# Performance work log

Measured on AMD Instinct MI355X. Metric: run time of the kernel, lower is better.

Reference implementation:

```python
import jax, jax.numpy as jnp
import numpy as np

EMB = 2048
HEADS = 16


def setup_inputs() -> dict:
    key = jax.random.key(0)
    k_x, k_wqkv, k_bqkv, k_wo, k_bo = jax.random.split(key, 5)
    B, S, E = 2, 2048, EMB
    x = jax.random.normal(k_x, (B, S, E), dtype=jnp.float32)
    # nn.Linear weights stored as (in, out) for x @ W + b convention
    W_qkv = jax.random.normal(k_wqkv, (E, 3 * E), dtype=jnp.float32) * 0.02
    b_qkv = jax.random.normal(k_bqkv, (3 * E,), dtype=jnp.float32) * 0.02
    W_out = jax.random.normal(k_wo, (E, E), dtype=jnp.float32) * 0.02
    b_out = jax.random.normal(k_bo, (E,), dtype=jnp.float32) * 0.02
    return {"x": x, "W_qkv": W_qkv, "b_qkv": b_qkv, "W_out": W_out, "b_out": b_out}


def reference(x, W_qkv, b_qkv, W_out, b_out):
    B, S, E = x.shape
    H = HEADS
    dh = E // H
    # QKV projection: (B,S,3E)
    qkv = x @ W_qkv + b_qkv
    # Faithful to torch: reshape (B,S,H,3*dh) THEN split -> interleaved per-head q/k/v
    qkv = qkv.reshape(B, S, H, 3 * dh).transpose(0, 2, 1, 3)  # (B,H,S,3*dh)
    q, k, v = jnp.split(qkv, 3, axis=-1)  # each (B,H,S,dh)
    q = q / jnp.asarray(dh, q.dtype) ** 0.5
    scores = jnp.einsum('bhqd,bhkd->bhqk', q, k)  # (B,H,S,S)
    weights = jax.nn.softmax(scores, axis=-1)
    attn = jnp.einsum('bhqk,bhkd->bhqd', weights, v)  # (B,H,S,dh)
    attn = attn.transpose(0, 2, 1, 3).reshape(B, S, E)
    return attn @ W_out + b_out
```

## Files before the change

kernel.cpp:

```cpp
#include <hip/hip_runtime.h>
#include <type_traits>
#include <utility>

#define DI __device__ __forceinline__

typedef unsigned short u16;
typedef float f32x4 __attribute__((ext_vector_type(4)));
typedef float f32x16 __attribute__((ext_vector_type(16)));
typedef short s16x8 __attribute__((ext_vector_type(8)));
typedef __bf16 bf16x8 __attribute__((ext_vector_type(8)));

template <typename V, typename = void>
struct mfma_ok : std::false_type {};
template <typename V>
struct mfma_ok<V, std::void_t<decltype(__builtin_amdgcn_mfma_f32_16x16x32_bf16(
    std::declval<V>(), std::declval<V>(), std::declval<f32x4>(), 0, 0, 0))>>
    : std::true_type {};
using frag_t = std::conditional_t<mfma_ok<bf16x8>::value, bf16x8, s16x8>;

union U128 {
  int4 i;
  frag_t f;
  u16 s[8];
};

DI f32x4 mfma16(const U128& a, const U128& b, f32x4 c) {
  return __builtin_amdgcn_mfma_f32_16x16x32_bf16(a.f, b.f, c, 0, 0, 0);
}
DI f32x16 mfma32(const U128& a, const U128& b, f32x16 c) {
  return __builtin_amdgcn_mfma_f32_32x32x16_bf16(a.f, b.f, c, 0, 0, 0);
}

DI u16 f2b(float x) {
  union { float f; unsigned u; } v; v.f = x;
  unsigned r = v.u + 0x7FFFu + ((v.u >> 16) & 1u);
  return (u16)(r >> 16);
}

DI unsigned pk2bf(float a, float b) {
  unsigned short ua = __builtin_bit_cast(unsigned short, (__bf16)a);
  unsigned short ub = __builtin_bit_cast(unsigned short, (__bf16)b);
  return (unsigned)ua | ((unsigned)ub << 16);
}

#if __has_builtin(__builtin_amdgcn_exp2f)
#define EXP2F __builtin_amdgcn_exp2f
#else
#define EXP2F exp2f
#endif

DI void plswap(unsigned& lo, unsigned& hi) {
  asm("v_permlane32_swap_b32 %0, %1" : "+v"(lo), "+v"(hi));
}

typedef __attribute__((address_space(1))) void gas_t;
typedef __attribute__((address_space(3))) void las_t;
DI void gll16(const void* g, void* l) {
  __builtin_amdgcn_global_load_lds((gas_t*)g, (las_t*)l, 16, 0, 0);
}

#define QSCALE 0.12751791437603762f

DI void transpose_tile(const float* __restrict__ in, u16* __restrict__ out,
                       int R, int C, int bx, int by, int t, u16 (*Tb)[68]) {
  long r0 = (long)by * 64, c0 = (long)bx * 64;
  int cq = (t & 15) * 4, rr = t >> 4;
#pragma unroll
  for (int it = 0; it < 4; ++it) {
    int r = rr + it * 16;
    float4 v = *(const float4*)(in + (r0 + r) * C + c0 + cq);
    Tb[r][cq + 0] = f2b(v.x); Tb[r][cq + 1] = f2b(v.y);
    Tb[r][cq + 2] = f2b(v.z); Tb[r][cq + 3] = f2b(v.w);
  }
  __syncthreads();
#pragma unroll
  for (int it = 0; it < 2; ++it) {
    int ci = it * 256 + t;
    int cc = ci >> 3, ch = ci & 7, rb = ch * 8;
    unsigned p0 = Tb[rb + 0][cc] | ((unsigned)Tb[rb + 1][cc] << 16);
    unsigned p1 = Tb[rb + 2][cc] | ((unsigned)Tb[rb + 3][cc] << 16);
    unsigned p2 = Tb[rb + 4][cc] | ((unsigned)Tb[rb + 5][cc] << 16);
    unsigned p3 = Tb[rb + 6][cc] | ((unsigned)Tb[rb + 7][cc] << 16);
    *(int4*)(out + (c0 + cc) * R + r0 + rb) = make_int4(p0, p1, p2, p3);
  }
}

__global__ __launch_bounds__(256) void k_pre(const float* __restrict__ x,
                                             u16* __restrict__ xb,
                                             const float* __restrict__ Wqkv,
                                             u16* __restrict__ wqkvt) {
  __shared__ __attribute__((aligned(16))) u16 Tb[64][68];
  int bid = blockIdx.x, t = threadIdx.x;
  if (bid < 8192) {
    int i = bid * 256 + t;
    float4 v = ((const float4*)x)[i];
    ushort4 o;
    o.x = f2b(v.x); o.y = f2b(v.y); o.z = f2b(v.z); o.w = f2b(v.w);
    ((ushort4*)xb)[i] = o;
    return;
  }
  int idx = bid - 8192;
  transpose_tile(Wqkv, wqkvt, 2048, 6144, idx % 96, idx / 96, t, Tb);
}

template <int MODE>
__global__ __launch_bounds__(256, 4) void k_gemm_bt(const u16* __restrict__ A,
                                                    const u16* __restrict__ Bt,
                                                    const float* __restrict__ bias,
                                                    void* __restrict__ Cout,
                                                    u16* __restrict__ qb,
                                                    u16* __restrict__ kbv,
                                                    u16* __restrict__ vt,
                                                    int n_off,
                                                    int M, int N, int K) {
  __shared__ __attribute__((aligned(16))) u16 SM[16384];
  u16* As = SM;
  u16* Bs = SM + 8192;
  int t = threadIdx.x;
  int lane = t & 63, w = t >> 6, quad = lane >> 4, l15 = lane & 15;
  long m0 = (long)blockIdx.y * 128, n0 = n_off + (long)blockIdx.x * 128;
  int wr = (w >> 1) * 64, wc = (w & 1) * 64;
  int sw = l15 & 7;
  f32x4 acc[4][4] = {};
  for (int k0 = 0; k0 < K; k0 += 64) {
    __syncthreads();
#pragma unroll
    for (int it = 0; it < 4; ++it) {
      int ci = it * 256 + t;
      int row = ci >> 3, cl = (ci & 7) ^ (row & 7);
      gll16(A + (m0 + row) * K + k0 + cl * 8, As + ci * 8);
      gll16(Bt + (n0 + row) * K + k0 + cl * 8, Bs + ci * 8);
    }
    __syncthreads();
#pragma unroll
    for (int kk = 0; kk < 2; ++kk) {
      U128 a[4], b[4];
#pragma unroll
      for (int i = 0; i < 4; ++i)
        a[i].i = *(const int4*)(As + (wr + i * 16 + l15) * 64 + (((kk * 4 + quad) ^ sw) << 3));
#pragma unroll
      for (int j = 0; j < 4; ++j)
        b[j].i = *(const int4*)(Bs + (wc + j * 16 + l15) * 64 + (((kk * 4 + quad) ^ sw) << 3));
#pragma unroll
      for (int i = 0; i < 4; ++i)
#pragma unroll
        for (int j = 0; j < 4; ++j)
          acc[i][j] = mfma16(a[i], b[j], acc[i][j]);
    }
  }
  float bj[4];
#pragma unroll
  for (int j = 0; j < 4; ++j) bj[j] = bias[n0 + wc + j * 16 + l15];

  int hidx = (int)(n0 / 384);
  int rsel = (int)(n0 - hidx * 384) >> 7;

  if (MODE == 1 && rsel == 2) {
    __syncthreads();
#pragma unroll
    for (int i = 0; i < 4; ++i)
#pragma unroll
      for (int rr2 = 0; rr2 < 4; ++rr2) {
        int m = wr + i * 16 + quad * 4 + rr2;
#pragma unroll
        for (int j = 0; j < 4; ++j)
          SM[m * 128 + wc + j * 16 + l15] = f2b(acc[i][j][rr2] + bj[j]);
      }
    __syncthreads();
    int bidx = (int)(m0 >> 11), s0 = (int)(m0 & 2047);
    u16* vrow = vt + (long)(bidx * 16 + hidx) * 128 * 2048 + s0;
#pragma unroll
    for (int it = 0; it < 8; ++it) {
      int ci = it * 256 + t;
      int d = ci & 127, sb = (ci >> 7) * 8;
      unsigned p0 = SM[(sb + 0) * 128 + d] | ((unsigned)SM[(sb + 1) * 128 + d] << 16);
      unsigned p1 = SM[(sb + 2) * 128 + d] | ((unsigned)SM[(sb + 3) * 128 + d] << 16);
      unsigned p2 = SM[(sb + 4) * 128 + d] | ((unsigned)SM[(sb + 5) * 128 + d] << 16);
      unsigned p3 = SM[(sb + 6) * 128 + d] | ((unsigned)SM[(sb + 7) * 128 + d] << 16);
      *(int4*)(vrow + (long)d * 2048 + sb) = make_int4(p0, p1, p2, p3);
    }
    return;
  }

  u16* route = (MODE == 1) ? (rsel == 0 ? qb : kbv) : nullptr;

#pragma unroll
  for (int i = 0; i < 4; ++i) {
#pragma unroll
    for (int rr2 = 0; rr2 < 4; ++rr2) {
      long row = m0 + wr + i * 16 + quad * 4 + rr2;
#pragma unroll
      for (int j = 0; j < 4; ++j) {
        float v = acc[i][j][rr2] + bj[j];
        if (MODE == 1) {
          if (rsel == 0) v *= QSCALE;
          int bidx = (int)(row >> 11), s = (int)(row & 2047);
          long obase = ((long)(bidx * 16 + hidx) * 2048 + s) * 128;
          int dh = wc + j * 16 + l15;
          unsigned pb = f2b(v);
          unsigned other = __shfl_xor(pb, 1);
          if (!(l15 & 1))
            ((unsigned*)route)[(obase + dh) >> 1] = pb | (other << 16);
        } else {
          long col = n0 + wc + j * 16 + l15;
          unsigned bits = __float_as_uint(v);
          unsigned other = __shfl_xor(bits, 1);
          if (!(l15 & 1)) {
            uint2 pr; pr.x = bits; pr.y = other;
            *(uint2*)((float*)Cout + row * N + col) = pr;
          }
        }
      }
    }
  }
}

__global__ __launch_bounds__(256, 2) void k_flash(const u16* __restrict__ qb,
                                                  const u16* __restrict__ kb,
                                                  const u16* __restrict__ vt,
                                                  u16* __restrict__ attn,
                                                  const float* __restrict__ Wout,
                                                  u16* __restrict__ woutt) {
  __shared__ __attribute__((aligned(16))) u16 Ks[2][64 * 128];
  __shared__ __attribute__((aligned(16))) u16 Vts[2][128 * 64];
  if (blockIdx.y >= 32) {
    u16 (*Tb)[68] = (u16(*)[68])(&Ks[0][0]);
    int u = (blockIdx.y - 32) * 16 + blockIdx.x;
    transpose_tile(Wout, woutt, 2048, 2048, u & 31, u >> 5, threadIdx.x, Tb);
    return;
  }
  int t = threadIdx.x;
  int lane = t & 63, w = t >> 6, l31 = lane & 31, h = lane >> 5;
  int q0 = blockIdx.x * 128 + w * 32;
  int bh = blockIdx.y, b = bh >> 4, hd = bh & 15;

  const u16* qbase = qb + ((long)bh * 2048 + q0 + l31) * 128;
  U128 qf[8];
#pragma unroll
  for (int dht = 0; dht < 8; ++dht)
    qf[dht].i = *(const int4*)(qbase + dht * 16 + h * 8);
  __syncthreads();

  f32x16 O[4] = {};
  float ls0 = 0.f, ls1 = 0.f, ls2 = 0.f, ls3 = 0.f;
  const u16* kbh = kb + (long)bh * 2048 * 128;
  long vbase = (long)bh * 128 * 2048;

  unsigned swx = (unsigned)(((l31 & 7) << 3) ^ (h << 3));
  unsigned kinv = ((unsigned)l31 << 7) ^ swx;
  unsigned vinv = ((unsigned)l31 << 6) ^ swx;

  auto stage = [&](int buf, int k0) {
#pragma unroll
    for (int it = 0; it < 4; ++it) {
      int ci = it * 256 + t;
      int key = ci >> 4, cp = ci & 15, cl = cp ^ (key & 7);
      gll16(kbh + (long)(k0 + key) * 128 + cl * 8, &Ks[buf][0] + ci * 8);
    }
#pragma unroll
    for (int it = 0; it < 4; ++it) {
      int ci = it * 256 + t;
      int d = ci >> 3, cp = ci & 7, cl = cp ^ (d & 7);
      gll16(vt + vbase + (long)d * 2048 + k0 + cl * 8, &Vts[buf][0] + ci * 8);
    }
  };

  stage(0, 0);
  int cur = 0;
  for (int k0 = 0; k0 < 2048; k0 += 64) {
    if (k0 + 64 < 2048) {
      stage(cur ^ 1, k0 + 64);
      asm volatile("s_waitcnt vmcnt(8)" ::: "memory");
    } else {
      asm volatile("s_waitcnt vmcnt(0)" ::: "memory");
    }
    __builtin_amdgcn_s_barrier();
    asm volatile("" ::: "memory");
    const u16* KbT = &Ks[cur][0];
    const u16* VbT = &Vts[cur][0];

    f32x16 St0 = {}, St1 = {};
    __builtin_amdgcn_s_setprio(1);
#pragma unroll
    for (int dht = 0; dht < 8; ++dht) {
      U128 kf;
      kf.i = *(const int4*)(KbT + (kinv ^ (unsigned)(dht << 4)));
      St0 = mfma32(kf, qf[dht], St0);
    }
#pragma unroll
    for (int dht = 0; dht < 8; ++dht) {
      U128 kf;
      kf.i = *(const int4*)(KbT + (kinv ^ (unsigned)(dht << 4)) + 4096);
      St1 = mfma32(kf, qf[dht], St1);
    }
    __builtin_amdgcn_s_setprio(0);

    auto pv = [&](int kt, const U128& pfk) {
#pragma unroll
      for (int dht = 0; dht < 4; ++dht) {
        U128 vf;
        vf.i = *(const int4*)(VbT + (vinv ^ (unsigned)(kt << 4)) + dht * 2048);
        O[dht] = mfma32(vf, pfk, O[dht]);
      }
    };
    auto mkpf = [&](const float* p) {
      unsigned w0 = pk2bf(p[0], p[1]);
      unsigned w1 = pk2bf(p[2], p[3]);
      unsigned w2 = pk2bf(p[4], p[5]);
      unsigned w3 = pk2bf(p[6], p[7]);
      plswap(w0, w2);
      plswap(w1, w3);
      U128 r; r.i = make_int4(w0, w1, w2, w3);
      return r;
    };

    float p0[16];
#pragma unroll
    for (int r = 0; r < 16; r += 4) {
      p0[r + 0] = EXP2F(St0[r + 0]); ls0 += p0[r + 0];
      p0[r + 1] = EXP2F(St0[r + 1]); ls1 += p0[r + 1];
      p0[r + 2] = EXP2F(St0[r + 2]); ls2 += p0[r + 2];
      p0[r + 3] = EXP2F(St0[r + 3]); ls3 += p0[r + 3];
    }
    U128 pf0 = mkpf(&p0[0]);
    U128 pf1 = mkpf(&p0[8]);

    pv(0, pf0);

    float p1[16];
#pragma unroll
    for (int r = 0; r < 8; r += 4) {
      p1[r + 0] = EXP2F(St1[r + 0]); ls0 += p1[r + 0];
      p1[r + 1] = EXP2F(St1[r + 1]); ls1 += p1[r + 1];
      p1[r + 2] = EXP2F(St1[r + 2]); ls2 += p1[r + 2];
      p1[r + 3] = EXP2F(St1[r + 3]); ls3 += p1[r + 3];
    }
    pv(1, pf1);

#pragma unroll
    for (int r = 8; r < 16; r += 4) {
      p1[r + 0] = EXP2F(St1[r + 0]); ls0 += p1[r + 0];
      p1[r + 1] = EXP2F(St1[r + 1]); ls1 += p1[r + 1];
      p1[r + 2] = EXP2F(St1[r + 2]); ls2 += p1[r + 2];
      p1[r + 3] = EXP2F(St1[r + 3]); ls3 += p1[r + 3];
    }
    U128 pf2 = mkpf(&p1[0]);
    U128 pf3 = mkpf(&p1[8]);

    __builtin_amdgcn_s_setprio(1);
    pv(2, pf2);
    pv(3, pf3);
    __builtin_amdgcn_s_setprio(0);

    asm volatile("" ::: "memory");
    __builtin_amdgcn_s_barrier();
    cur ^= 1;
  }

  float lsum = (ls0 + ls1) + (ls2 + ls3);
  float ltot = lsum + __shfl_xor(lsum, 32);
  float inv = 1.f / ltot;
  long orow = (long)b * 2048 + q0 + l31;
  u16* ob = attn + orow * 2048 + hd * 128;
#pragma unroll
  for (int dht = 0; dht < 4; ++dht)
#pragma unroll
    for (int g = 0; g < 4; ++g) {
      int dh = dht * 32 + g * 8 + h * 4;
      float v0 = O[dht][4 * g + 0] * inv, v1 = O[dht][4 * g + 1] * inv;
      float v2 = O[dht][4 * g + 2] * inv, v3 = O[dht][4 * g + 3] * inv;
      uint2 pkd;
      pkd.x = pk2bf(v0, v1);
      pkd.y = pk2bf(v2, v3);
      *(uint2*)(ob + dh) = pkd;
    }
}

extern "C" void kernel_launch(void* const* d_in, const int* in_sizes, int n_in,
                              void* d_out, int out_size, void* d_ws, size_t ws_size,
                              hipStream_t stream) {
  const float* x    = (const float*)d_in[0];
  const float* Wqkv = (const float*)d_in[1];
  const float* bqkv = (const float*)d_in[2];
  const float* Wout = (const float*)d_in[3];
  const float* bout = (const float*)d_in[4];
  float* out = (float*)d_out;
  char* ws = (char*)d_ws;

  if (ws_size < 75497472u) return;

  u16* xb    = (u16*)d_out;
  u16* wqkvt = (u16*)(ws);
  u16* qbuf  = (u16*)(ws + 25165824);
  u16* kbuf  = (u16*)(ws + 41943040);
  u16* vtb   = (u16*)(ws + 58720256);
  u16* woutt = (u16*)(ws);
  u16* attnb = (u16*)(ws + 8388608);

  k_pre<<<11264, 256, 0, stream>>>(x, xb, Wqkv, wqkvt);
  k_gemm_bt<1><<<dim3(48, 32), 256, 0, stream>>>(xb, wqkvt, bqkv, nullptr,
                                                 qbuf, kbuf, vtb, 0, 4096, 6144, 2048);
  k_flash<<<dim3(16, 96), 256, 0, stream>>>(qbuf, kbuf, vtb, attnb, Wout, woutt);
  k_gemm_bt<0><<<dim3(16, 32), 256, 0, stream>>>(attnb, woutt, bout, out,
                                                 nullptr, nullptr, nullptr, 0, 4096, 2048, 2048);
}
```

Measured before the change: 364.8 us.

## Tile V-transpose layout and double flash block size to 512 threads

The QKV GEMM epilogue now writes V-transposed data in 128x128 tiles (d-major within each sequence tile) through a padded, transposed shared-memory staging buffer, so each thread's global store is contiguous and the LDS reads are conflict-reduced 32-bit words. The flash kernel is changed to 512-thread blocks covering 256 queries, halving the grid so each K/V tile staged in LDS is shared by eight waves instead of four, and its V loads follow the new tiled layout. The Wout transpose side-blocks process two tiles per block. More waves per block may reduce occupancy flexibility and raise per-block LDS pressure.

```diff
diff --git a/kernel.cpp b/kernel.cpp
--- a/kernel.cpp
+++ b/kernel.cpp
@@ -113,7 +113,7 @@
                                                     u16* __restrict__ vt,
                                                     int n_off,
                                                     int M, int N, int K) {
-  __shared__ __attribute__((aligned(16))) u16 SM[16384];
+  __shared__ __attribute__((aligned(16))) u16 SM[16640];
   u16* As = SM;
   u16* Bs = SM + 8192;
   int t = threadIdx.x;
@@ -164,20 +164,20 @@
         int m = wr + i * 16 + quad * 4 + rr2;
 #pragma unroll
         for (int j = 0; j < 4; ++j)
-          SM[m * 128 + wc + j * 16 + l15] = f2b(acc[i][j][rr2] + bj[j]);
+          SM[(wc + j * 16 + l15) * 130 + m] = f2b(acc[i][j][rr2] + bj[j]);
       }
     __syncthreads();
-    int bidx = (int)(m0 >> 11), s0 = (int)(m0 & 2047);
-    u16* vrow = vt + (long)(bidx * 16 + hidx) * 128 * 2048 + s0;
+    int bidx = (int)(m0 >> 11);
+    int stile = (int)((m0 & 2047) >> 7);
+    u16* vtile = vt + (long)(bidx * 16 + hidx) * 262144 + stile * 16384;
+    const unsigned* sm32 = (const unsigned*)SM;
 #pragma unroll
     for (int it = 0; it < 8; ++it) {
       int ci = it * 256 + t;
-      int d = ci & 127, sb = (ci >> 7) * 8;
-      unsigned p0 = SM[(sb + 0) * 128 + d] | ((unsigned)SM[(sb + 1) * 128 + d] << 16);
-      unsigned p1 = SM[(sb + 2) * 128 + d] | ((unsigned)SM[(sb + 3) * 128 + d] << 16);
-      unsigned p2 = SM[(sb + 4) * 128 + d] | ((unsigned)SM[(sb + 5) * 128 + d] << 16);
-      unsigned p3 = SM[(sb + 6) * 128 + d] | ((unsigned)SM[(sb + 7) * 128 + d] << 16);
-      *(int4*)(vrow + (long)d * 2048 + sb) = make_int4(p0, p1, p2, p3);
+      int d = ci >> 4, sb = (ci & 15) * 8;
+      int base = (d * 130 + sb) >> 1;
+      *(int4*)(vtile + d * 128 + sb) =
+          make_int4(sm32[base], sm32[base + 1], sm32[base + 2], sm32[base + 3]);
     }
     return;
   }
@@ -215,7 +215,7 @@
   }
 }
 
-__global__ __launch_bounds__(256, 2) void k_flash(const u16* __restrict__ qb,
+__global__ __launch_bounds__(512, 2) void k_flash(const u16* __restrict__ qb,
                                                   const u16* __restrict__ kb,
                                                   const u16* __restrict__ vt,
                                                   u16* __restrict__ attn,
@@ -224,14 +224,15 @@
   __shared__ __attribute__((aligned(16))) u16 Ks[2][64 * 128];
   __shared__ __attribute__((aligned(16))) u16 Vts[2][128 * 64];
   if (blockIdx.y >= 32) {
-    u16 (*Tb)[68] = (u16(*)[68])(&Ks[0][0]);
-    int u = (blockIdx.y - 32) * 16 + blockIdx.x;
-    transpose_tile(Wout, woutt, 2048, 2048, u & 31, u >> 5, threadIdx.x, Tb);
+    int half = threadIdx.x >> 8, tt = threadIdx.x & 255;
+    u16 (*Tb)[68] = (u16(*)[68])(&Ks[0][0] + half * 64 * 68);
+    int u = ((blockIdx.y - 32) * 8 + blockIdx.x) * 2 + half;
+    transpose_tile(Wout, woutt, 2048, 2048, u & 31, u >> 5, tt, Tb);
     return;
   }
   int t = threadIdx.x;
   int lane = t & 63, w = t >> 6, l31 = lane & 31, h = lane >> 5;
-  int q0 = blockIdx.x * 128 + w * 32;
+  int q0 = blockIdx.x * 256 + w * 32;
   int bh = blockIdx.y, b = bh >> 4, hd = bh & 15;
 
   const u16* qbase = qb + ((long)bh * 2048 + q0 + l31) * 128;
@@ -244,7 +245,7 @@
   f32x16 O[4] = {};
   float ls0 = 0.f, ls1 = 0.f, ls2 = 0.f, ls3 = 0.f;
   const u16* kbh = kb + (long)bh * 2048 * 128;
-  long vbase = (long)bh * 128 * 2048;
+  long vbase = (long)bh * 262144;
 
   unsigned swx = (unsigned)(((l31 & 7) << 3) ^ (h << 3));
   unsigned kinv = ((unsigned)l31 << 7) ^ swx;
@@ -252,16 +253,17 @@
 
   auto stage = [&](int buf, int k0) {
 #pragma unroll
-    for (int it = 0; it < 4; ++it) {
-      int ci = it * 256 + t;
+    for (int it = 0; it < 2; ++it) {
+      int ci = it * 512 + t;
       int key = ci >> 4, cp = ci & 15, cl = cp ^ (key & 7);
       gll16(kbh + (long)(k0 + key) * 128 + cl * 8, &Ks[buf][0] + ci * 8);
     }
 #pragma unroll
-    for (int it = 0; it < 4; ++it) {
-      int ci = it * 256 + t;
+    for (int it = 0; it < 2; ++it) {
+      int ci = it * 512 + t;
       int d = ci >> 3, cp = ci & 7, cl = cp ^ (d & 7);
-      gll16(vt + vbase + (long)d * 2048 + k0 + cl * 8, &Vts[buf][0] + ci * 8);
+      gll16(vt + vbase + ((k0 >> 7) << 14) + d * 128 + (k0 & 64) + cl * 8,
+            &Vts[buf][0] + ci * 8);
     }
   };
 
@@ -270,7 +272,7 @@
   for (int k0 = 0; k0 < 2048; k0 += 64) {
     if (k0 + 64 < 2048) {
       stage(cur ^ 1, k0 + 64);
-      asm volatile("s_waitcnt vmcnt(8)" ::: "memory");
+      asm volatile("s_waitcnt vmcnt(4)" ::: "memory");
     } else {
       asm volatile("s_waitcnt vmcnt(0)" ::: "memory");
     }
@@ -400,7 +402,7 @@
   k_pre<<<11264, 256, 0, stream>>>(x, xb, Wqkv, wqkvt);
   k_gemm_bt<1><<<dim3(48, 32), 256, 0, stream>>>(xb, wqkvt, bqkv, nullptr,
                                                  qbuf, kbuf, vtb, 0, 4096, 6144, 2048);
-  k_flash<<<dim3(16, 96), 256, 0, stream>>>(qbuf, kbuf, vtb, attnb, Wout, woutt);
+  k_flash<<<dim3(8, 96), 512, 0, stream>>>(qbuf, kbuf, vtb, attnb, Wout, woutt);
   k_gemm_bt<0><<<dim3(16, 32), 256, 0, stream>>>(attnb, woutt, bout, out,
                                                  nullptr, nullptr, nullptr, 0, 4096, 2048, 2048);
 }
```

New measurement: 373.6 us. 1.02x slower.
